# Kernel optimization log

Measured on AMD Instinct MI355X. Metric: run time of the kernel, lower is better.

## Reference

```python
import jax, jax.numpy as jnp
import numpy as np

T, C, H, E, TOPK = 8192, 1024, 4096, 8, 2
ALPHA = 0.01


def setup_inputs() -> dict:
    key = jax.random.key(0)
    ks = jax.random.split(key, 10)
    std = 0.01
    return {
        "x": jax.random.normal(ks[0], (T, C), dtype=jnp.float32),
        "gate_w": jax.random.normal(ks[1], (E, C), dtype=jnp.float32) * std,  # nn.init.normal_(std=0.01)
        "wg": jax.random.normal(ks[2], (E, C, H), dtype=jnp.float32) * 0.02,
        "wu": jax.random.normal(ks[3], (E, C, H), dtype=jnp.float32) * 0.02,
        "wd": jax.random.normal(ks[4], (E, H, C), dtype=jnp.float32) * 0.02,
        "swg": jax.random.normal(ks[5], (C, H), dtype=jnp.float32) * 0.02,
        "swu": jax.random.normal(ks[6], (C, H), dtype=jnp.float32) * 0.02,
        "swd": jax.random.normal(ks[7], (H, C), dtype=jnp.float32) * 0.02,
        "shared_scale": jnp.ones((1,), dtype=jnp.float32) * 0.5,
    }


def _swiglu(h, g, u, d):
    # SwiGLU FFN: W_down( silu(W_gate x) * W_up x )
    return (jax.nn.silu(h @ g) * (h @ u)) @ d


def reference(x, gate_w, wg, wu, wd, swg, swu, swd, shared_scale):
    # ---- gate (top-k softmax routing) ----
    logits = x @ gate_w.T                       # [T, E]
    scores = jax.nn.softmax(logits, axis=-1)    # [T, E]
    topk_w, topk_idx = jax.lax.top_k(scores, TOPK)
    topk_w = topk_w / jnp.sum(topk_w, axis=-1, keepdims=True)

    # per-token combine weight for each expert: sum_k w_k * [idx_k == e]  -> [T, E]
    comb = jnp.zeros((x.shape[0], E), dtype=x.dtype)
    comb = comb.at[jnp.arange(x.shape[0])[:, None], topk_idx].add(topk_w)

    # ---- routed experts (dispatch-FFN-combine, expressed as masked dense combine) ----
    y = jnp.zeros_like(x)
    for e in range(E):  # fixed small expert count
        y = y + comb[:, e:e + 1] * _swiglu(x, wg[e], wu[e], wd[e])

    # ---- shared expert ----
    y = y + shared_scale * _swiglu(x, swg, swu, swd)

    # ---- load-balancing aux loss (training mode) ----
    onehot = jax.nn.one_hot(topk_idx.reshape(-1), E, dtype=x.dtype)  # [T*K, E]
    ce = onehot.mean(axis=0)
    fi = ce * E
    Pi = scores.mean(axis=0)
    aux_loss = jnp.sum(Pi * fi) * ALPHA
    return y, aux_loss
```

## Files before the change

kernel.cpp:

```cpp
#include <hip/hip_runtime.h>
#include <hip/hip_bf16.h>
#include <stdint.h>

#define T_TOK 8192
#define CDIM  1024
#define HDIM  4096
#define NEXP  8
#define TOPK_ 2
#define GT_MAX 72
#define UT_MAX 104
#define GROWS_MAX (GT_MAX * 256)

typedef __attribute__((ext_vector_type(8))) short short8;
typedef __attribute__((ext_vector_type(4))) float f32x4;

__device__ __forceinline__ void gload16(const short* g, short* l) {
  __builtin_amdgcn_global_load_lds(
      (const __attribute__((address_space(1))) unsigned int*)(g),
      (__attribute__((address_space(3))) unsigned int*)(l), 16, 0, 0);
}

__global__ __launch_bounds__(256) void gate_kernel(
    const float* __restrict__ x, const float* __restrict__ gw,
    int* __restrict__ tokinfo, float* __restrict__ tokw,
    int* __restrict__ bcnt, float* __restrict__ spart)
{
  const int wid = threadIdx.x >> 6, lane = threadIdx.x & 63;
  const int t = blockIdx.x * 4 + wid;
  float acc[NEXP];
#pragma unroll
  for (int e = 0; e < NEXP; ++e) acc[e] = 0.f;
  const float4* xr = (const float4*)x + (size_t)t * (CDIM / 4);
  const float4* gw4 = (const float4*)gw;
#pragma unroll
  for (int i = 0; i < CDIM / 256; ++i) {
    const float4 xv = xr[lane + 64 * i];
#pragma unroll
    for (int e = 0; e < NEXP; ++e) {
      const float4 gv = gw4[e * (CDIM / 4) + lane + 64 * i];
      acc[e] += xv.x * gv.x + xv.y * gv.y + xv.z * gv.z + xv.w * gv.w;
    }
  }
#pragma unroll
  for (int off = 32; off > 0; off >>= 1) {
#pragma unroll
    for (int e = 0; e < NEXP; ++e) acc[e] += __shfl_xor(acc[e], off);
  }
  float mx = acc[0];
#pragma unroll
  for (int e = 1; e < NEXP; ++e) mx = fmaxf(mx, acc[e]);
  float p[NEXP]; float s = 0.f;
#pragma unroll
  for (int e = 0; e < NEXP; ++e) { p[e] = __expf(acc[e] - mx); s += p[e]; }
  const float inv = 1.f / s;
#pragma unroll
  for (int e = 0; e < NEXP; ++e) p[e] *= inv;
  float v0 = p[0]; int i0 = 0;
#pragma unroll
  for (int e = 1; e < NEXP; ++e) if (p[e] > v0) { v0 = p[e]; i0 = e; }
  float v1 = -1.f; int i1 = 0;
#pragma unroll
  for (int e = 0; e < NEXP; ++e) if (e != i0 && p[e] > v1) { v1 = p[e]; i1 = e; }

  __shared__ float sp[4][NEXP];
  __shared__ int   se[4][2];
  __shared__ float swt[4][2];
  if (lane == 0) {
#pragma unroll
    for (int e = 0; e < NEXP; ++e) sp[wid][e] = p[e];
    const float wn = 1.f / (v0 + v1);
    se[wid][0] = i0; se[wid][1] = i1;
    swt[wid][0] = v0 * wn; swt[wid][1] = v1 * wn;
  }
  __syncthreads();
  if (threadIdx.x == 0) {
    int cnt[NEXP];
#pragma unroll
    for (int e = 0; e < NEXP; ++e) cnt[e] = 0;
#pragma unroll
    for (int tt = 0; tt < 4; ++tt) {
      const int e0 = se[tt][0], e1 = se[tt][1];
      const int r0 = cnt[e0]++; const int r1 = cnt[e1]++;
      tokinfo[blockIdx.x * 4 + tt] = e0 | (e1 << 3) | (r0 << 6) | (r1 << 10);
      ((float2*)tokw)[blockIdx.x * 4 + tt] = make_float2(swt[tt][0], swt[tt][1]);
    }
#pragma unroll
    for (int e = 0; e < NEXP; ++e) bcnt[blockIdx.x * NEXP + e] = cnt[e];
  }
  if (threadIdx.x < NEXP)
    spart[blockIdx.x * NEXP + threadIdx.x] =
        sp[0][threadIdx.x] + sp[1][threadIdx.x] + sp[2][threadIdx.x] + sp[3][threadIdx.x];
}

__global__ __launch_bounds__(512) void scan_kernel(
    const int* __restrict__ bcnt, int* __restrict__ boff, int* __restrict__ ecnt,
    const float* __restrict__ spart, float* __restrict__ aux_out,
    int* __restrict__ pad_off, int* __restrict__ tile_map, int* __restrict__ ntiles)
{
  const int w = threadIdx.x >> 6, l = threadIdx.x & 63;
  int run = 0;
#pragma unroll 4
  for (int c = 0; c < (T_TOK / 4) / 64; ++c) {
    const int b = c * 64 + l;
    const int v = bcnt[b * NEXP + w];
    int sc = v;
#pragma unroll
    for (int off = 1; off < 64; off <<= 1) {
      const int t = __shfl_up(sc, off);
      if (l >= off) sc += t;
    }
    boff[b * NEXP + w] = run + sc - v;
    run += __shfl(sc, 63);
  }
  if (l == 0) ecnt[w] = run;
  float fs = 0.f;
  for (int c = 0; c < (T_TOK / 4) / 64; ++c) fs += spart[(c * 64 + l) * NEXP + w];
#pragma unroll
  for (int off = 32; off > 0; off >>= 1) fs += __shfl_xor(fs, off);
  __shared__ float pis[NEXP];
  __shared__ int cs[NEXP];
  if (l == 0) { pis[w] = fs; cs[w] = run; }
  __syncthreads();
  if (threadIdx.x == 0) {
    float aux = 0.f;
#pragma unroll
    for (int e = 0; e < NEXP; ++e) {
      const float Pi = pis[e] / (float)T_TOK;
      const float ce = (float)cs[e] / (float)(T_TOK * TOPK_);
      aux += Pi * ce * (float)NEXP;
    }
    aux_out[0] = aux * 0.01f;
    ecnt[8] = T_TOK;
    int acc = 0, nt = 0;
    for (int e = 0; e < NEXP; ++e) {
      pad_off[e] = acc;
      const int te = (cs[e] + 255) >> 8;
      for (int t = 0; t < te; ++t) { tile_map[nt] = e | ((t * 256) << 4); ++nt; }
      acc += te * 256;
    }
    ntiles[0] = nt;
    for (int t = 0; t < T_TOK / 256; ++t) { tile_map[nt] = 8 | ((t * 256) << 4); ++nt; }
    ntiles[1] = nt;
  }
}

__global__ __launch_bounds__(256) void scatter_kernel(
    const int* __restrict__ tokinfo, const float* __restrict__ tokw,
    const int* __restrict__ boff, const int* __restrict__ pad_off,
    int* __restrict__ grows, float* __restrict__ gww)
{
  const int t = blockIdx.x * 256 + threadIdx.x;
  const int info = tokinfo[t];
  const int e0 = info & 7, e1 = (info >> 3) & 7;
  const int r0 = (info >> 6) & 15, r1 = (info >> 10) & 15;
  const int b = t >> 2;
  const float2 wv = ((const float2*)tokw)[t];
  const int g0 = pad_off[e0] + boff[b * NEXP + e0] + r0;
  grows[g0] = t; gww[g0] = wv.x;
  const int g1 = pad_off[e1] + boff[b * NEXP + e1] + r1;
  grows[g1] = t; gww[g1] = wv.y;
}

__global__ __launch_bounds__(256) void cvt_x_kernel(const float* __restrict__ x,
                                                    __hip_bfloat16* __restrict__ xb)
{
  const int i = blockIdx.x * 256 + threadIdx.x;
  const float4 v = ((const float4*)x)[i];
  union { __hip_bfloat16 h[4]; uint2 u; } o;
  o.h[0] = __float2bfloat16(v.x); o.h[1] = __float2bfloat16(v.y);
  o.h[2] = __float2bfloat16(v.z); o.h[3] = __float2bfloat16(v.w);
  ((uint2*)xb)[i] = o.u;
}

struct TD { const float* src; __hip_bfloat16* dst; int N; int nsh; int M; };
struct TB { TD d[27]; };
__global__ __launch_bounds__(256) void tbatch_kernel(TB tb)
{
  const int m = blockIdx.x >> 12;
  const int t = blockIdx.x & 4095;
  const TD td = tb.d[m];
  const int n0 = (t & ((1 << td.nsh) - 1)) << 5;
  const int m0 = (t >> td.nsh) << 5;
  __shared__ float tile[32][33];
  const int tx = threadIdx.x & 31, ty = threadIdx.x >> 5;
#pragma unroll
  for (int i = 0; i < 4; ++i)
    tile[ty + 8 * i][tx] = td.src[(size_t)(m0 + ty + 8 * i) * td.N + n0 + tx];
  __syncthreads();
#pragma unroll
  for (int i = 0; i < 4; ++i)
    td.dst[(size_t)(n0 + ty + 8 * i) * td.M + m0 + tx] = __float2bfloat16(tile[tx][ty + 8 * i]);
}

template <int OP>
__global__ __launch_bounds__(512, 2) void gemm_pipe_kernel(
    const __hip_bfloat16* __restrict__ Abase,
    const __hip_bfloat16* __restrict__ B0mat,
    const __hip_bfloat16* __restrict__ B1mat,
    __hip_bfloat16* __restrict__ midout,
    float* __restrict__ y,
    const int* __restrict__ rowlist, const float* __restrict__ roww,
    const int* __restrict__ ecnt, const int* __restrict__ tile_map,
    const int* __restrict__ ntiles, const float* __restrict__ ssc,
    int mode, int tile_base)
{
  constexpr int K = (OP == 1) ? CDIM : HDIM;
  constexpr int NT = K / 32;
  __shared__ __align__(16) short lds[65536];

  int ti = blockIdx.y + tile_base;
  if (mode == 2) ti += ntiles[0];
  const int hi = (mode == 1) ? ntiles[0] : ntiles[1];
  if (ti >= hi) return;
  const int tm = tile_map[ti];
  const int e = tm & 15, rb = tm >> 4;
  const int rows_valid = ecnt[e] - rb;
  const int gbmid = (int)blockIdx.y * 256;
  const int glist = ti * 256;

  const int t = threadIdx.x, l = t & 63, w = t >> 6;
  const int sr = t >> 2;
  const int csrc = (t & 3) ^ ((t >> 3) & 3);
  const int n0 = blockIdx.x * ((OP == 1) ? 128 : 256);

  const short *pA0, *pA1, *pB0, *pB1;
  if (OP == 1) {
    int r0g, r1g;
    if (e == 8) { r0g = rb + sr; r1g = rb + 128 + sr; }
    else {
      const int c0 = sr < rows_valid ? sr : rows_valid - 1;
      const int c1 = (128 + sr) < rows_valid ? (128 + sr) : rows_valid - 1;
      r0g = rowlist[glist + c0]; r1g = rowlist[glist + c1];
    }
    pA0 = (const short*)Abase + (size_t)r0g * K + csrc * 8;
    pA1 = (const short*)Abase + (size_t)r1g * K + csrc * 8;
    const int br0 = sr, br1 = 128 + sr;
    const int s0 = (br0 >> 4) & 1, s1 = (br1 >> 4) & 1;
    const int h0 = n0 + (br0 >> 5) * 16 + (br0 & 15);
    const int h1 = n0 + (br1 >> 5) * 16 + (br1 & 15);
    pB0 = (const short*)(s0 ? B1mat : B0mat) + (size_t)e * CDIM * HDIM + (size_t)h0 * K + csrc * 8;
    pB1 = (const short*)(s1 ? B1mat : B0mat) + (size_t)e * CDIM * HDIM + (size_t)h1 * K + csrc * 8;
  } else {
    pA0 = (const short*)Abase + (size_t)(gbmid + sr) * K + csrc * 8;
    pA1 = (const short*)Abase + (size_t)(gbmid + 128 + sr) * K + csrc * 8;
    const short* bb = (const short*)B0mat + (size_t)e * CDIM * HDIM;
    pB0 = bb + (size_t)(n0 + sr) * K + csrc * 8;
    pB1 = bb + (size_t)(n0 + 128 + sr) * K + csrc * 8;
  }
  short* dstA = lds + w * 512;
  short* dstB = lds + 32768 + w * 512;

  const int wr = w >> 2, wc = w & 3;
  const int cswz = (l >> 1) & 3;
  const int chunk = (((l >> 4) ^ cswz) << 3);
  const int afb = wr * 4096 + (l & 15) * 32 + chunk;
  const int bfb = 32768 + (wc >> 1) * 4096 + ((wc & 1) * 64 + (l & 15)) * 32 + chunk;

  f32x4 acc[8][4];
#pragma unroll
  for (int i = 0; i < 8; ++i)
#pragma unroll
    for (int j = 0; j < 4; ++j) acc[i][j] = (f32x4){0.f, 0.f, 0.f, 0.f};

#define STAGE_A(q) { const int s8_ = ((q) & 3) * 8192; \
    gload16(pA0 + (q) * 32, dstA + s8_); \
    gload16(pA1 + (q) * 32, dstA + s8_ + 4096); }
#define STAGE_B(q) { const int s8_ = ((q) & 3) * 8192; \
    gload16(pB0 + (q) * 32, dstB + s8_); \
    gload16(pB1 + (q) * 32, dstB + s8_ + 4096); }

  STAGE_A(0) STAGE_B(0) STAGE_A(1) STAGE_B(1)

  short8 af[8], bf[4];
  for (int q = 0; q < NT; ++q) {
    const int s8 = (q & 3) * 8192;
    asm volatile("s_waitcnt vmcnt(4)" ::: "memory");
    __syncthreads();
    if (q + 2 < NT) STAGE_A(q + 2)
#pragma unroll
    for (int mi = 0; mi < 4; ++mi) af[mi] = *(const short8*)(lds + s8 + afb + mi * 512);
#pragma unroll
    for (int ni = 0; ni < 4; ++ni) bf[ni] = *(const short8*)(lds + s8 + bfb + ni * 512);
    __builtin_amdgcn_s_setprio(1);
#pragma unroll
    for (int mi = 0; mi < 4; ++mi)
#pragma unroll
      for (int ni = 0; ni < 4; ++ni)
        acc[mi][ni] = __builtin_amdgcn_mfma_f32_16x16x32_bf16(af[mi], bf[ni], acc[mi][ni], 0, 0, 0);
    __builtin_amdgcn_s_setprio(0);
    __syncthreads();
    if (q + 2 < NT) STAGE_B(q + 2)
#pragma unroll
    for (int mi = 4; mi < 8; ++mi) af[mi] = *(const short8*)(lds + s8 + afb + mi * 512);
    __builtin_amdgcn_s_setprio(1);
#pragma unroll
    for (int mi = 4; mi < 8; ++mi)
#pragma unroll
      for (int ni = 0; ni < 4; ++ni)
        acc[mi][ni] = __builtin_amdgcn_mfma_f32_16x16x32_bf16(af[mi], bf[ni], acc[mi][ni], 0, 0, 0);
    __builtin_amdgcn_s_setprio(0);
  }
#undef STAGE_A
#undef STAGE_B

  const int rl = (l >> 4) * 4, cl = l & 15;
  if (OP == 1) {
#pragma unroll
    for (int mi = 0; mi < 8; ++mi) {
#pragma unroll
      for (int j = 0; j < 4; ++j) {
        const int rlocal = wr * 128 + mi * 16 + rl + j;
        if (rlocal < rows_valid) {
          __hip_bfloat16* mp = midout + (size_t)(gbmid + rlocal) * HDIM;
#pragma unroll
          for (int jj = 0; jj < 2; ++jj) {
            const float g = acc[mi][jj * 2][j], u = acc[mi][jj * 2 + 1][j];
            const float sv = g / (1.f + __expf(-g));
            mp[n0 + (wc * 2 + jj) * 16 + cl] = __float2bfloat16(sv * u);
          }
        }
      }
    }
  } else {
    const float ss = ssc[0];
#pragma unroll
    for (int mi = 0; mi < 8; ++mi) {
#pragma unroll
      for (int j = 0; j < 4; ++j) {
        const int rlocal = wr * 128 + mi * 16 + rl + j;
        if (rlocal < rows_valid) {
          int tok; float wgt;
          if (e == 8) { tok = rb + rlocal; wgt = ss; }
          else { tok = rowlist[glist + rlocal]; wgt = roww[glist + rlocal]; }
          float* yp = y + (size_t)tok * CDIM + n0 + wc * 64 + cl;
#pragma unroll
          for (int ni = 0; ni < 4; ++ni)
            unsafeAtomicAdd(yp + ni * 16, wgt * acc[mi][ni][j]);
        }
      }
    }
  }
}

extern "C" void kernel_launch(void* const* d_in, const int* in_sizes, int n_in,
                              void* d_out, int out_size, void* d_ws, size_t ws_size,
                              hipStream_t stream)
{
  const float* x   = (const float*)d_in[0];
  const float* gw  = (const float*)d_in[1];
  const float* wg  = (const float*)d_in[2];
  const float* wu  = (const float*)d_in[3];
  const float* wd  = (const float*)d_in[4];
  const float* swg = (const float*)d_in[5];
  const float* swu = (const float*)d_in[6];
  const float* swd = (const float*)d_in[7];
  const float* ssc = (const float*)d_in[8];
  float* y = (float*)d_out;

  auto al = [](size_t v) { return (v + 255) & ~(size_t)255; };
  char* ws = (char*)d_ws;
  size_t off = 0;
  __hip_bfloat16* xb = (__hip_bfloat16*)(ws + off); off += al((size_t)T_TOK * CDIM * 2);
  int*   tokinfo = (int*)(ws + off);   off += al((size_t)T_TOK * 4);
  float* tokw    = (float*)(ws + off); off += al((size_t)T_TOK * 8);
  int*   bcnt    = (int*)(ws + off);   off += al((size_t)(T_TOK / 4) * NEXP * 4);
  int*   boffb   = (int*)(ws + off);   off += al((size_t)(T_TOK / 4) * NEXP * 4);
  float* spart   = (float*)(ws + off); off += al((size_t)(T_TOK / 4) * NEXP * 4);
  int*   ecnt    = (int*)(ws + off);   off += 256;
  int*   pad_off = (int*)(ws + off);   off += 256;
  int*   ntiles  = (int*)(ws + off);   off += 256;
  int*   tile_map= (int*)(ws + off);   off += al((size_t)UT_MAX * 4);
  int*   grows   = (int*)(ws + off);   off += al((size_t)GROWS_MAX * 4);
  float* gww     = (float*)(ws + off); off += al((size_t)GROWS_MAX * 4);

  const size_t WMAT = (size_t)CDIM * HDIM;
  __hip_bfloat16* wg9 = (__hip_bfloat16*)(ws + off); off += 9 * WMAT * 2;
  __hip_bfloat16* wu9 = (__hip_bfloat16*)(ws + off); off += 9 * WMAT * 2;
  __hip_bfloat16* wd9 = (__hip_bfloat16*)(ws + off); off += 9 * WMAT * 2;
  __hip_bfloat16* mid = (__hip_bfloat16*)(ws + off);
  const size_t mid_avail = (ws_size > off) ? (ws_size - off) : 0;
  const size_t TILE_B = (size_t)256 * HDIM * 2;

  hipMemsetAsync(y, 0, (size_t)(T_TOK * CDIM + 1) * sizeof(float), stream);
  gate_kernel<<<T_TOK / 4, 256, 0, stream>>>(x, gw, tokinfo, tokw, bcnt, spart);
  scan_kernel<<<1, 512, 0, stream>>>(bcnt, boffb, ecnt, spart, y + (size_t)T_TOK * CDIM,
                                     pad_off, tile_map, ntiles);
  scatter_kernel<<<T_TOK / 256, 256, 0, stream>>>(tokinfo, tokw, boffb, pad_off, grows, gww);
  cvt_x_kernel<<<T_TOK * CDIM / 4 / 256, 256, 0, stream>>>(x, xb);

  TB tb;
  for (int e = 0; e < 8; ++e) {
    tb.d[e]      = TD{wg + e * WMAT, wg9 + e * WMAT, HDIM, 7, CDIM};
    tb.d[8 + e]  = TD{wu + e * WMAT, wu9 + e * WMAT, HDIM, 7, CDIM};
    tb.d[16 + e] = TD{wd + e * WMAT, wd9 + e * WMAT, CDIM, 5, HDIM};
  }
  tb.d[24] = TD{swg, wg9 + 8 * WMAT, HDIM, 7, CDIM};
  tb.d[25] = TD{swu, wu9 + 8 * WMAT, HDIM, 7, CDIM};
  tb.d[26] = TD{swd, wd9 + 8 * WMAT, CDIM, 5, HDIM};
  tbatch_kernel<<<27 * 4096, 256, 0, stream>>>(tb);

  if (mid_avail >= (size_t)UT_MAX * TILE_B) {
    gemm_pipe_kernel<1><<<dim3(HDIM / 128, UT_MAX), 512, 0, stream>>>(
        xb, wg9, wu9, mid, nullptr, grows, gww, ecnt, tile_map, ntiles, ssc, 0, 0);
    gemm_pipe_kernel<2><<<dim3(CDIM / 256, UT_MAX), 512, 0, stream>>>(
        mid, wd9, nullptr, nullptr, y, grows, gww, ecnt, tile_map, ntiles, ssc, 0, 0);
  } else if (mid_avail >= (size_t)GT_MAX * TILE_B) {
    gemm_pipe_kernel<1><<<dim3(HDIM / 128, GT_MAX), 512, 0, stream>>>(
        xb, wg9, wu9, mid, nullptr, grows, gww, ecnt, tile_map, ntiles, ssc, 1, 0);
    gemm_pipe_kernel<2><<<dim3(CDIM / 256, GT_MAX), 512, 0, stream>>>(
        mid, wd9, nullptr, nullptr, y, grows, gww, ecnt, tile_map, ntiles, ssc, 1, 0);
    gemm_pipe_kernel<1><<<dim3(HDIM / 128, 32), 512, 0, stream>>>(
        xb, wg9, wu9, mid, nullptr, grows, gww, ecnt, tile_map, ntiles, ssc, 2, 0);
    gemm_pipe_kernel<2><<<dim3(CDIM / 256, 32), 512, 0, stream>>>(
        mid, wd9, nullptr, nullptr, y, grows, gww, ecnt, tile_map, ntiles, ssc, 2, 0);
  } else {
    int CH = (int)(mid_avail / TILE_B);
    if (CH < 1) CH = 1;
    for (int c0 = 0; c0 < GT_MAX; c0 += CH) {
      const int g = (GT_MAX - c0) < CH ? (GT_MAX - c0) : CH;
      gemm_pipe_kernel<1><<<dim3(HDIM / 128, g), 512, 0, stream>>>(
          xb, wg9, wu9, mid, nullptr, grows, gww, ecnt, tile_map, ntiles, ssc, 1, c0);
      gemm_pipe_kernel<2><<<dim3(CDIM / 256, g), 512, 0, stream>>>(
          mid, wd9, nullptr, nullptr, y, grows, gww, ecnt, tile_map, ntiles, ssc, 1, c0);
    }
    for (int c0 = 0; c0 < 32; c0 += CH) {
      const int g = (32 - c0) < CH ? (32 - c0) : CH;
      gemm_pipe_kernel<1><<<dim3(HDIM / 128, g), 512, 0, stream>>>(
          xb, wg9, wu9, mid, nullptr, grows, gww, ecnt, tile_map, ntiles, ssc, 2, c0);
      gemm_pipe_kernel<2><<<dim3(CDIM / 256, g), 512, 0, stream>>>(
          mid, wd9, nullptr, nullptr, y, grows, gww, ecnt, tile_map, ntiles, ssc, 2, c0);
    }
  }
}
```

Baseline: 1.090 ms.

## Split down-projection GEMM four ways along K and drop the mid-loop barrier

The down-projection GEMM (OP 2) now launches with a grid z-dimension of 4. Each block covers a 1024-wide K slice at offset blockIdx.z*1024, with a fixed 32-iteration loop, so it runs four times as many blocks for better CU occupancy. This assumes the OP 2 epilogue already accumulates into y atomically; if it does not, the partial sums would be lost. The main loop also goes from two barriers per iteration to one. All eight A fragments are loaded before the MFMAs, the second __syncthreads is removed, and the last iteration drains with vmcnt(0). The trade-off is more atomic traffic on y and less separation between LDS buffer reuse and the reads of that buffer.

```diff
diff --git a/kernel.cpp b/kernel.cpp
--- a/kernel.cpp
+++ b/kernel.cpp
@@ -205,7 +205,7 @@
     int mode, int tile_base)
 {
   constexpr int K = (OP == 1) ? CDIM : HDIM;
-  constexpr int NT = K / 32;
+  constexpr int NT = 32;
   __shared__ __align__(16) short lds[65536];
 
   int ti = blockIdx.y + tile_base;
@@ -217,6 +217,7 @@
   const int rows_valid = ecnt[e] - rb;
   const int gbmid = (int)blockIdx.y * 256;
   const int glist = ti * 256;
+  const int kbase = (OP == 2) ? (int)blockIdx.z * 1024 : 0;
 
   const int t = threadIdx.x, l = t & 63, w = t >> 6;
   const int sr = t >> 2;
@@ -241,11 +242,11 @@
     pB0 = (const short*)(s0 ? B1mat : B0mat) + (size_t)e * CDIM * HDIM + (size_t)h0 * K + csrc * 8;
     pB1 = (const short*)(s1 ? B1mat : B0mat) + (size_t)e * CDIM * HDIM + (size_t)h1 * K + csrc * 8;
   } else {
-    pA0 = (const short*)Abase + (size_t)(gbmid + sr) * K + csrc * 8;
-    pA1 = (const short*)Abase + (size_t)(gbmid + 128 + sr) * K + csrc * 8;
+    pA0 = (const short*)Abase + (size_t)(gbmid + sr) * K + kbase + csrc * 8;
+    pA1 = (const short*)Abase + (size_t)(gbmid + 128 + sr) * K + kbase + csrc * 8;
     const short* bb = (const short*)B0mat + (size_t)e * CDIM * HDIM;
-    pB0 = bb + (size_t)(n0 + sr) * K + csrc * 8;
-    pB1 = bb + (size_t)(n0 + 128 + sr) * K + csrc * 8;
+    pB0 = bb + (size_t)(n0 + sr) * K + kbase + csrc * 8;
+    pB1 = bb + (size_t)(n0 + 128 + sr) * K + kbase + csrc * 8;
   }
   short* dstA = lds + w * 512;
   short* dstB = lds + 32768 + w * 512;
@@ -274,13 +275,19 @@
   short8 af[8], bf[4];
   for (int q = 0; q < NT; ++q) {
     const int s8 = (q & 3) * 8192;
-    asm volatile("s_waitcnt vmcnt(4)" ::: "memory");
-    __syncthreads();
+    if (q == NT - 1) {
+      asm volatile("s_waitcnt vmcnt(0)\n\ts_barrier" ::: "memory");
+    } else {
+      asm volatile("s_waitcnt vmcnt(4)\n\ts_barrier" ::: "memory");
+    }
+    __builtin_amdgcn_sched_barrier(0);
     if (q + 2 < NT) STAGE_A(q + 2)
 #pragma unroll
     for (int mi = 0; mi < 4; ++mi) af[mi] = *(const short8*)(lds + s8 + afb + mi * 512);
 #pragma unroll
     for (int ni = 0; ni < 4; ++ni) bf[ni] = *(const short8*)(lds + s8 + bfb + ni * 512);
+#pragma unroll
+    for (int mi = 4; mi < 8; ++mi) af[mi] = *(const short8*)(lds + s8 + afb + mi * 512);
     __builtin_amdgcn_s_setprio(1);
 #pragma unroll
     for (int mi = 0; mi < 4; ++mi)
@@ -288,10 +295,7 @@
       for (int ni = 0; ni < 4; ++ni)
         acc[mi][ni] = __builtin_amdgcn_mfma_f32_16x16x32_bf16(af[mi], bf[ni], acc[mi][ni], 0, 0, 0);
     __builtin_amdgcn_s_setprio(0);
-    __syncthreads();
     if (q + 2 < NT) STAGE_B(q + 2)
-#pragma unroll
-    for (int mi = 4; mi < 8; ++mi) af[mi] = *(const short8*)(lds + s8 + afb + mi * 512);
     __builtin_amdgcn_s_setprio(1);
 #pragma unroll
     for (int mi = 4; mi < 8; ++mi)
@@ -402,16 +406,16 @@
   if (mid_avail >= (size_t)UT_MAX * TILE_B) {
     gemm_pipe_kernel<1><<<dim3(HDIM / 128, UT_MAX), 512, 0, stream>>>(
         xb, wg9, wu9, mid, nullptr, grows, gww, ecnt, tile_map, ntiles, ssc, 0, 0);
-    gemm_pipe_kernel<2><<<dim3(CDIM / 256, UT_MAX), 512, 0, stream>>>(
+    gemm_pipe_kernel<2><<<dim3(CDIM / 256, UT_MAX, 4), 512, 0, stream>>>(
         mid, wd9, nullptr, nullptr, y, grows, gww, ecnt, tile_map, ntiles, ssc, 0, 0);
   } else if (mid_avail >= (size_t)GT_MAX * TILE_B) {
     gemm_pipe_kernel<1><<<dim3(HDIM / 128, GT_MAX), 512, 0, stream>>>(
         xb, wg9, wu9, mid, nullptr, grows, gww, ecnt, tile_map, ntiles, ssc, 1, 0);
-    gemm_pipe_kernel<2><<<dim3(CDIM / 256, GT_MAX), 512, 0, stream>>>(
+    gemm_pipe_kernel<2><<<dim3(CDIM / 256, GT_MAX, 4), 512, 0, stream>>>(
         mid, wd9, nullptr, nullptr, y, grows, gww, ecnt, tile_map, ntiles, ssc, 1, 0);
     gemm_pipe_kernel<1><<<dim3(HDIM / 128, 32), 512, 0, stream>>>(
         xb, wg9, wu9, mid, nullptr, grows, gww, ecnt, tile_map, ntiles, ssc, 2, 0);
-    gemm_pipe_kernel<2><<<dim3(CDIM / 256, 32), 512, 0, stream>>>(
+    gemm_pipe_kernel<2><<<dim3(CDIM / 256, 32, 4), 512, 0, stream>>>(
         mid, wd9, nullptr, nullptr, y, grows, gww, ecnt, tile_map, ntiles, ssc, 2, 0);
   } else {
     int CH = (int)(mid_avail / TILE_B);
@@ -420,14 +424,14 @@
       const int g = (GT_MAX - c0) < CH ? (GT_MAX - c0) : CH;
       gemm_pipe_kernel<1><<<dim3(HDIM / 128, g), 512, 0, stream>>>(
           xb, wg9, wu9, mid, nullptr, grows, gww, ecnt, tile_map, ntiles, ssc, 1, c0);
-      gemm_pipe_kernel<2><<<dim3(CDIM / 256, g), 512, 0, stream>>>(
+      gemm_pipe_kernel<2><<<dim3(CDIM / 256, g, 4), 512, 0, stream>>>(
           mid, wd9, nullptr, nullptr, y, grows, gww, ecnt, tile_map, ntiles, ssc, 1, c0);
     }
     for (int c0 = 0; c0 < 32; c0 += CH) {
       const int g = (32 - c0) < CH ? (32 - c0) : CH;
       gemm_pipe_kernel<1><<<dim3(HDIM / 128, g), 512, 0, stream>>>(
           xb, wg9, wu9, mid, nullptr, grows, gww, ecnt, tile_map, ntiles, ssc, 2, c0);
-      gemm_pipe_kernel<2><<<dim3(CDIM / 256, g), 512, 0, stream>>>(
+      gemm_pipe_kernel<2><<<dim3(CDIM / 256, g, 4), 512, 0, stream>>>(
           mid, wd9, nullptr, nullptr, y, grows, gww, ecnt, tile_map, ntiles, ssc, 2, c0);
     }
   }
```

Result: faster. 1.040 ms (-4.6%).
